# Kernel tuning notes

Hardware: AMD Instinct MI355X
Metric: run time of the kernel (lower is better)

The kernel has to match this reference:

```python
import jax, jax.numpy as jnp
import numpy as np

B, R, A, S, F, N = 2, 1, 16, 14, 1024, 512  # batch, num_rx, num_rx_ant, ofdm_symbols, fft_size, num_effective_sc
D = S * N  # flattened time-frequency dim that C acts on


def setup_inputs() -> dict:
    key = jax.random.key(0)
    k0, k1, k2, k3 = jax.random.split(key, 4)
    scale = 1.0 / np.sqrt(D).astype(np.float32)
    x_re = jax.random.normal(k0, (B, R, A, S, F), jnp.float32)
    x_im = jax.random.normal(k1, (B, R, A, S, F), jnp.float32)
    C_re = jax.random.normal(k2, (D, D), jnp.float32) * scale
    C_im = jax.random.normal(k3, (D, D), jnp.float32) * scale
    # unique, sorted effective-subcarrier indices (as in an OFDM ResourceGrid)
    sc_ind = jnp.asarray(np.sort(np.random.default_rng(0).choice(F, N, replace=False)), jnp.int32)
    return {"x_re": x_re, "x_im": x_im, "C_re": C_re, "C_im": C_im, "sc_ind": sc_ind}


def reference(x_re, x_im, C_re, C_im, sc_ind):
    x = jax.lax.complex(x_re, x_im)            # [B,R,A,S,F] complex64
    C = jax.lax.complex(C_re, C_im)            # [D,D]
    y = jnp.take(x, sc_ind, axis=-1)           # gather effective subcarriers -> [B,R,A,S,N]
    b, r, a, s, n = y.shape
    yf = y.reshape(b, r, a, s * n)             # flatten_last_dims(y, 2)
    # multiply_from_right with adjoint: yf @ C^H
    yf = jnp.einsum('brad,ed->brae', yf, jnp.conj(C))
    y = yf.reshape(b, r, a, s, n)
    # scatter back into full fft_size grid (unique indices -> set == scatter_nd on zeros)
    out = jnp.zeros((b, r, a, s, F), y.dtype).at[..., sc_ind].set(y)
    return jnp.stack([out.real, out.imag])     # [2,B,R,A,S,F] (real, imag)
```

## Files before the change

kernel.cpp:

```cpp
#include <hip/hip_runtime.h>
#include <hip/hip_bf16.h>

#define B_ 2
#define R_ 1
#define A_ 16
#define S_ 14
#define F_ 1024
#define N_ 512
#define D_ (S_*N_)
#define M_ (B_*R_*A_)
#define KK_ (2*D_)
#define BE 64
#define ETILES (D_/BE)

typedef __attribute__((ext_vector_type(8))) short bf16x8;
typedef __attribute__((ext_vector_type(4))) float f32x4;

static __device__ inline short f2bf(float f) {
    __hip_bfloat16 h = __float2bfloat16(f);
    return *reinterpret_cast<short*>(&h);
}
static __device__ inline float bf2f(short s) {
    unsigned int u = ((unsigned int)(unsigned short)s) << 16;
    return __uint_as_float(u);
}

#define LDSP(p) ((__attribute__((address_space(3))) void*)(p))
#define GLBP(p) ((const __attribute__((address_space(1))) void*)(p))

__global__ void prep_kernel(const float* __restrict__ xr, const float* __restrict__ xi,
                            const int* __restrict__ sc, short* __restrict__ Ap) {
    int idx = blockIdx.x * blockDim.x + threadIdx.x;
    if (idx >= 64 * KK_) return;
    int k = idx % KK_;
    int r = idx / KK_;
    int m = r & 31;
    int half = (k >= D_) ? 1 : 0;
    int d = half ? (k - D_) : k;
    int s = d >> 9;
    int n = d & 511;
    int f = sc[n];
    const float* base = (r < 32) ? (half ? xi : xr) : (half ? xr : xi);
    float v = base[(m * S_ + s) * F_ + f];
    if (r >= 32 && half) v = -v;
    Ap[((size_t)(k >> 3) * 64 + r) * 8 + (k & 7)] = f2bf(v);
}

__global__ void zero_kernel(float4* __restrict__ out, int n4) {
    int i = blockIdx.x * blockDim.x + threadIdx.x;
    if (i < n4) out[i] = make_float4(0.f, 0.f, 0.f, 0.f);
}

__global__ __launch_bounds__(256) void gemm_wasync(
    const short* __restrict__ Ap,
    const float* __restrict__ Cre, const float* __restrict__ Cim,
    short* __restrict__ part_all)
{
    constexpr int KSPLIT = 28;
    constexpr int KBLK = KK_ / KSPLIT;
    constexpr int NCH  = KBLK / 32;
    __shared__ float Bl[4][3][16 * 32];
    __shared__ short Al[4][3][64 * 32];

    const int etile = blockIdx.x;
    const int ks    = blockIdx.y;
    const int tid   = threadIdx.x;
    const int wave  = tid >> 6;
    const int lane  = tid & 63;
    const int l16   = lane & 15;
    const int kg    = lane >> 4;

    const float* Cp = (ks < 14) ? Cre : Cim;
    const int kc = (ks % 14) * KBLK;
    const int ka = ks * KBLK;

    const int U0 = lane, U1 = 64 + lane;
    const float* bsrc0 = Cp + (size_t)(etile * 64 + wave * 16 + (U0 >> 3)) * D_
                            + kc + ((U0 & 7) ^ ((U0 >> 3) & 7)) * 4;
    const float* bsrc1 = Cp + (size_t)(etile * 64 + wave * 16 + (U1 >> 3)) * D_
                            + kc + ((U1 & 7) ^ ((U1 >> 3) & 7)) * 4;
    const short* asrc = Ap + (size_t)(ka >> 3) * 512 + lane * 8;

#define WAITV(n) asm volatile("s_waitcnt vmcnt(" #n ")" ::: "memory")
#define STAGE(cc) do { \
        int bb = (cc) % 3; \
        __builtin_amdgcn_global_load_lds(GLBP(bsrc0 + (size_t)(cc) * 32), \
                                         LDSP(&Bl[wave][bb][lane * 4]), 16, 0, 0); \
        __builtin_amdgcn_global_load_lds(GLBP(bsrc1 + (size_t)(cc) * 32), \
                                         LDSP(&Bl[wave][bb][(64 + lane) * 4]), 16, 0, 0); \
        __builtin_amdgcn_global_load_lds(GLBP(asrc + (size_t)(cc) * 2048 + 0 * 512), \
                                         LDSP(&Al[wave][bb][lane * 8]), 16, 0, 0); \
        __builtin_amdgcn_global_load_lds(GLBP(asrc + (size_t)(cc) * 2048 + 1 * 512), \
                                         LDSP(&Al[wave][bb][(64 + lane) * 8]), 16, 0, 0); \
        __builtin_amdgcn_global_load_lds(GLBP(asrc + (size_t)(cc) * 2048 + 2 * 512), \
                                         LDSP(&Al[wave][bb][(128 + lane) * 8]), 16, 0, 0); \
        __builtin_amdgcn_global_load_lds(GLBP(asrc + (size_t)(cc) * 2048 + 3 * 512), \
                                         LDSP(&Al[wave][bb][(192 + lane) * 8]), 16, 0, 0); \
    } while (0)

    STAGE(0);
    STAGE(1);
    STAGE(2);

    f32x4 acc0 = {0.f,0.f,0.f,0.f}, acc1 = {0.f,0.f,0.f,0.f};
    f32x4 acc2 = {0.f,0.f,0.f,0.f}, acc3 = {0.f,0.f,0.f,0.f};

    const int swz  = l16 & 7;
    const int boff = l16 * 32;
    const int u0x = ((kg * 2 + 0) ^ swz) * 4;
    const int u1x = ((kg * 2 + 1) ^ swz) * 4;

    for (int c = 0; c < NCH; ++c) {
        if (c <= NCH - 3)      { WAITV(12); }
        else if (c == NCH - 2) { WAITV(6); }
        else                   { WAITV(0); }
        __builtin_amdgcn_sched_barrier(0);

        const int buf = c % 3;
        f32x4 b0 = *reinterpret_cast<const f32x4*>(&Bl[wave][buf][boff + u0x]);
        f32x4 b1 = *reinterpret_cast<const f32x4*>(&Bl[wave][buf][boff + u1x]);
        bf16x8 a0 = *reinterpret_cast<const bf16x8*>(&Al[wave][buf][(kg * 64 + 0 * 16 + l16) * 8]);
        bf16x8 a1 = *reinterpret_cast<const bf16x8*>(&Al[wave][buf][(kg * 64 + 1 * 16 + l16) * 8]);
        bf16x8 a2 = *reinterpret_cast<const bf16x8*>(&Al[wave][buf][(kg * 64 + 2 * 16 + l16) * 8]);
        bf16x8 a3 = *reinterpret_cast<const bf16x8*>(&Al[wave][buf][(kg * 64 + 3 * 16 + l16) * 8]);
        asm volatile("s_waitcnt lgkmcnt(0)" ::: "memory");
        __builtin_amdgcn_sched_barrier(0);

        if (c + 3 < NCH) STAGE(c + 3);
        __builtin_amdgcn_sched_barrier(0);

        bf16x8 bfv;
        bfv[0] = f2bf(b0.x); bfv[1] = f2bf(b0.y); bfv[2] = f2bf(b0.z); bfv[3] = f2bf(b0.w);
        bfv[4] = f2bf(b1.x); bfv[5] = f2bf(b1.y); bfv[6] = f2bf(b1.z); bfv[7] = f2bf(b1.w);
        acc0 = __builtin_amdgcn_mfma_f32_16x16x32_bf16(a0, bfv, acc0, 0, 0, 0);
        acc1 = __builtin_amdgcn_mfma_f32_16x16x32_bf16(a1, bfv, acc1, 0, 0, 0);
        acc2 = __builtin_amdgcn_mfma_f32_16x16x32_bf16(a2, bfv, acc2, 0, 0, 0);
        acc3 = __builtin_amdgcn_mfma_f32_16x16x32_bf16(a3, bfv, acc3, 0, 0, 0);
    }
#undef STAGE
#undef WAITV

    const int e_lane = etile * 64 + wave * 16 + l16;
    short* part = part_all + (size_t)ks * (64 * D_);
    #pragma unroll
    for (int mt = 0; mt < 4; ++mt) {
        f32x4 a = (mt == 0) ? acc0 : (mt == 1) ? acc1 : (mt == 2) ? acc2 : acc3;
        int rbase = mt * 16 + kg * 4;
        #pragma unroll
        for (int r = 0; r < 4; ++r)
            part[(size_t)(rbase + r) * D_ + e_lane] = f2bf(a[r]);
    }
}

template<int KSPLIT, int PARTIALS>
__global__ __launch_bounds__(256) void gemm_sync(
    const short* __restrict__ Ap,
    const float* __restrict__ Cre, const float* __restrict__ Cim,
    const int* __restrict__ sc,
    void* __restrict__ outp)
{
    constexpr int KBLK = KK_ / KSPLIT;
    constexpr int NCH  = KBLK / 32;
    __shared__ float Bls[3][64 * 32];
    __shared__ short Als[3][64 * 32];

    const int etile = blockIdx.x;
    const int ks    = blockIdx.y;
    const int tid   = threadIdx.x;
    const int wave  = tid >> 6;
    const int lane  = tid & 63;
    const int l16   = lane & 15;
    const int kg    = lane >> 4;

    const float* Cp = (ks < KSPLIT / 2) ? Cre : Cim;
    const int kc = (ks % (KSPLIT / 2)) * KBLK;
    const int ka = ks * KBLK;

    const float* bsrc[2];
    #pragma unroll
    for (int q = 0; q < 2; ++q) {
        int U = q * 256 + tid;
        int row = U >> 3;
        int u = (U & 7) ^ (row & 7);
        bsrc[q] = Cp + (size_t)(etile * BE + row) * D_ + kc + u * 4;
    }
    const short* asrc = Ap + ((size_t)(ka >> 3) * 64) * 8 + tid * 8;

#define STG(c) do { \
        int bf_ = (c) % 3; \
        __builtin_amdgcn_global_load_lds(GLBP(bsrc[0] + (size_t)(c) * 32), \
                                         LDSP(&Bls[bf_][(0 * 256 + tid) * 4]), 16, 0, 0); \
        __builtin_amdgcn_global_load_lds(GLBP(bsrc[1] + (size_t)(c) * 32), \
                                         LDSP(&Bls[bf_][(1 * 256 + tid) * 4]), 16, 0, 0); \
        __builtin_amdgcn_global_load_lds(GLBP(asrc + (size_t)(c) * 2048), \
                                         LDSP(&Als[bf_][tid * 8]), 16, 0, 0); \
    } while (0)

    STG(0);
    STG(1);

    f32x4 acc0 = {0.f,0.f,0.f,0.f}, acc1 = {0.f,0.f,0.f,0.f};
    f32x4 acc2 = {0.f,0.f,0.f,0.f}, acc3 = {0.f,0.f,0.f,0.f};

    const int row  = wave * 16 + l16;
    const int swz  = row & 7;
    const int boff = row * 32;
    const int u0 = ((kg * 2 + 0) ^ swz) * 4;
    const int u1 = ((kg * 2 + 1) ^ swz) * 4;

    for (int c = 0; c < NCH; ++c) {
        if (c < NCH - 1) asm volatile("s_waitcnt vmcnt(3)" ::: "memory");
        else             asm volatile("s_waitcnt vmcnt(0)" ::: "memory");
        __builtin_amdgcn_sched_barrier(0);
        __builtin_amdgcn_s_barrier();

        const int buf = c % 3;
        f32x4 b0 = *reinterpret_cast<const f32x4*>(&Bls[buf][boff + u0]);
        f32x4 b1 = *reinterpret_cast<const f32x4*>(&Bls[buf][boff + u1]);
        bf16x8 a0 = *reinterpret_cast<const bf16x8*>(&Als[buf][(kg * 64 + 0 * 16 + l16) * 8]);
        bf16x8 a1 = *reinterpret_cast<const bf16x8*>(&Als[buf][(kg * 64 + 1 * 16 + l16) * 8]);
        bf16x8 a2 = *reinterpret_cast<const bf16x8*>(&Als[buf][(kg * 64 + 2 * 16 + l16) * 8]);
        bf16x8 a3 = *reinterpret_cast<const bf16x8*>(&Als[buf][(kg * 64 + 3 * 16 + l16) * 8]);
        asm volatile("s_waitcnt lgkmcnt(0)" ::: "memory");
        __builtin_amdgcn_sched_barrier(0);
        __builtin_amdgcn_s_barrier();

        if (c + 2 < NCH) STG(c + 2);

        bf16x8 bfv;
        bfv[0] = f2bf(b0.x); bfv[1] = f2bf(b0.y); bfv[2] = f2bf(b0.z); bfv[3] = f2bf(b0.w);
        bfv[4] = f2bf(b1.x); bfv[5] = f2bf(b1.y); bfv[6] = f2bf(b1.z); bfv[7] = f2bf(b1.w);
        acc0 = __builtin_amdgcn_mfma_f32_16x16x32_bf16(a0, bfv, acc0, 0, 0, 0);
        acc1 = __builtin_amdgcn_mfma_f32_16x16x32_bf16(a1, bfv, acc1, 0, 0, 0);
        acc2 = __builtin_amdgcn_mfma_f32_16x16x32_bf16(a2, bfv, acc2, 0, 0, 0);
        acc3 = __builtin_amdgcn_mfma_f32_16x16x32_bf16(a3, bfv, acc3, 0, 0, 0);
    }
#undef STG

    const int e_lane = etile * BE + row;
    if (PARTIALS) {
        short* part = (short*)outp + (size_t)ks * (64 * D_);
        #pragma unroll
        for (int mt = 0; mt < 4; ++mt) {
            f32x4 a = (mt == 0) ? acc0 : (mt == 1) ? acc1 : (mt == 2) ? acc2 : acc3;
            int rbase = mt * 16 + kg * 4;
            #pragma unroll
            for (int r = 0; r < 4; ++r)
                part[(size_t)(rbase + r) * D_ + e_lane] = f2bf(a[r]);
        }
    } else {
        float* out = (float*)outp;
        int s = e_lane >> 9, n = e_lane & 511;
        int f = sc[n];
        #pragma unroll
        for (int mt = 0; mt < 4; ++mt) {
            f32x4 a = (mt == 0) ? acc0 : (mt == 1) ? acc1 : (mt == 2) ? acc2 : acc3;
            int rbase = mt * 16 + kg * 4;
            #pragma unroll
            for (int r = 0; r < 4; ++r) {
                int rr = rbase + r;
                int pp = rr >> 5, m = rr & 31;
                atomicAdd(&out[((pp * M_ + m) * S_ + s) * F_ + f], a[r]);
            }
        }
    }
}

template<int KSPLIT>
__global__ void reduce_kernel(const short* __restrict__ part, const int* __restrict__ sc,
                              float* __restrict__ out) {
    int t = blockIdx.x * blockDim.x + threadIdx.x;
    if (t >= 64 * D_ / 8) return;
    int base = t * 8;
    int e0 = base % D_;
    int r  = base / D_;
    float v[8] = {0.f,0.f,0.f,0.f,0.f,0.f,0.f,0.f};
    #pragma unroll
    for (int ksp = 0; ksp < KSPLIT; ++ksp) {
        bf16x8 x = *reinterpret_cast<const bf16x8*>(&part[(size_t)ksp * (64 * D_) + base]);
        #pragma unroll
        for (int j = 0; j < 8; ++j) v[j] += bf2f(x[j]);
    }
    int pp = r >> 5, m = r & 31, s = e0 >> 9, n0 = e0 & 511;
    float* ob = &out[((pp * M_ + m) * S_ + s) * F_];
    #pragma unroll
    for (int j = 0; j < 8; ++j) ob[sc[n0 + j]] = v[j];
}

extern "C" void kernel_launch(void* const* d_in, const int* in_sizes, int n_in,
                              void* d_out, int out_size, void* d_ws, size_t ws_size,
                              hipStream_t stream) {
    const float* xr  = (const float*)d_in[0];
    const float* xi  = (const float*)d_in[1];
    const float* Cre = (const float*)d_in[2];
    const float* Cim = (const float*)d_in[3];
    const int*   sc  = (const int*)d_in[4];
    float* out = (float*)d_out;

    short* Ap = (short*)d_ws;
    const size_t partOff = 2u * 1024u * 1024u;
    const size_t need28  = partOff + 28ull * 64 * D_ * 2;
    const size_t need16  = partOff + 16ull * 64 * D_ * 2;

    prep_kernel<<<dim3((64 * KK_ + 255) / 256), 256, 0, stream>>>(xr, xi, sc, Ap);
    zero_kernel<<<dim3((917504 / 4 + 255) / 256), 256, 0, stream>>>((float4*)out, 917504 / 4);

    const int rthreads = 64 * D_ / 8;
    if (ws_size >= need28) {
        short* part = (short*)((char*)d_ws + partOff);
        gemm_wasync<<<dim3(ETILES, 28), 256, 0, stream>>>(Ap, Cre, Cim, part);
        reduce_kernel<28><<<dim3((rthreads + 255) / 256), 256, 0, stream>>>(part, sc, out);
    } else if (ws_size >= need16) {
        short* part = (short*)((char*)d_ws + partOff);
        gemm_sync<16, 1><<<dim3(ETILES, 16), 256, 0, stream>>>(Ap, Cre, Cim, sc, part);
        reduce_kernel<16><<<dim3((rthreads + 255) / 256), 256, 0, stream>>>(part, sc, out);
    } else {
        gemm_sync<16, 0><<<dim3(ETILES, 16), 256, 0, stream>>>(Ap, Cre, Cim, sc, out);
    }
}
```

Baseline: 123.8 us.

## Replace LDS-staged split-K GEMM with register-prefetched GEMM and gather-based reduce

The main GEMM drops the global_load_lds staging through shared memory and instead prefetches C and A fragments straight into registers, several chunks deep. The K split goes from 28 to 14, halving the partial buffer traffic, and launch bounds ask for 2 blocks per CU. The reduce now writes the full output grid by looking up an inverse subcarrier map built by a new kernel, which removes the separate zero pass and the scattered writes. prep_kernel now reads each x element once and writes all four bf16 entries. Trade-offs: much higher register pressure from the prefetch arrays, fewer blocks in the GEMM grid, and gathered (non-vector) reads of the partials in the reduce.

```diff
diff --git a/kernel.cpp b/kernel.cpp
--- a/kernel.cpp
+++ b/kernel.cpp
@@ -31,19 +31,27 @@
 __global__ void prep_kernel(const float* __restrict__ xr, const float* __restrict__ xi,
                             const int* __restrict__ sc, short* __restrict__ Ap) {
     int idx = blockIdx.x * blockDim.x + threadIdx.x;
-    if (idx >= 64 * KK_) return;
-    int k = idx % KK_;
-    int r = idx / KK_;
-    int m = r & 31;
-    int half = (k >= D_) ? 1 : 0;
-    int d = half ? (k - D_) : k;
+    if (idx >= 32 * D_) return;
+    int d = idx % D_;
+    int m = idx / D_;
     int s = d >> 9;
     int n = d & 511;
     int f = sc[n];
-    const float* base = (r < 32) ? (half ? xi : xr) : (half ? xr : xi);
-    float v = base[(m * S_ + s) * F_ + f];
-    if (r >= 32 && half) v = -v;
-    Ap[((size_t)(k >> 3) * 64 + r) * 8 + (k & 7)] = f2bf(v);
+    float vr = xr[(m * S_ + s) * F_ + f];
+    float vi = xi[(m * S_ + s) * F_ + f];
+    int g1 = d >> 3, j = d & 7;
+    int g2 = (D_ + d) >> 3;
+    Ap[((size_t)g1 * 64 + m) * 8 + j]      = f2bf(vr);
+    Ap[((size_t)g1 * 64 + 32 + m) * 8 + j] = f2bf(vi);
+    Ap[((size_t)g2 * 64 + m) * 8 + j]      = f2bf(vi);
+    Ap[((size_t)g2 * 64 + 32 + m) * 8 + j] = f2bf(-vr);
+}
+
+__global__ void inv_kernel(const int* __restrict__ sc, int* __restrict__ inv) {
+    int t = threadIdx.x;
+    inv[t] = -1;
+    __syncthreads();
+    if (t < N_) inv[sc[t]] = t;
 }
 
 __global__ void zero_kernel(float4* __restrict__ out, int n4) {
@@ -51,16 +59,16 @@
     if (i < n4) out[i] = make_float4(0.f, 0.f, 0.f, 0.f);
 }
 
-__global__ __launch_bounds__(256) void gemm_wasync(
+__global__ __launch_bounds__(256, 2) void gemm_reg(
     const short* __restrict__ Ap,
     const float* __restrict__ Cre, const float* __restrict__ Cim,
     short* __restrict__ part_all)
 {
-    constexpr int KSPLIT = 28;
+    constexpr int KSPLIT = 14;
     constexpr int KBLK = KK_ / KSPLIT;
     constexpr int NCH  = KBLK / 32;
-    __shared__ float Bl[4][3][16 * 32];
-    __shared__ short Al[4][3][64 * 32];
+    constexpr int BD   = 5;
+    constexpr int AD   = 8;
 
     const int etile = blockIdx.x;
     const int ks    = blockIdx.y;
@@ -70,65 +78,51 @@
     const int l16   = lane & 15;
     const int kg    = lane >> 4;
 
-    const float* Cp = (ks < 14) ? Cre : Cim;
-    const int kc = (ks % 14) * KBLK;
+    const float* Cp = (ks < 7) ? Cre : Cim;
+    const int kc = (ks % 7) * KBLK;
     const int ka = ks * KBLK;
 
-    const int U0 = lane, U1 = 64 + lane;
-    const float* bsrc0 = Cp + (size_t)(etile * 64 + wave * 16 + (U0 >> 3)) * D_
-                            + kc + ((U0 & 7) ^ ((U0 >> 3) & 7)) * 4;
-    const float* bsrc1 = Cp + (size_t)(etile * 64 + wave * 16 + (U1 >> 3)) * D_
-                            + kc + ((U1 & 7) ^ ((U1 >> 3) & 7)) * 4;
-    const short* asrc = Ap + (size_t)(ka >> 3) * 512 + lane * 8;
-
-#define WAITV(n) asm volatile("s_waitcnt vmcnt(" #n ")" ::: "memory")
-#define STAGE(cc) do { \
-        int bb = (cc) % 3; \
-        __builtin_amdgcn_global_load_lds(GLBP(bsrc0 + (size_t)(cc) * 32), \
-                                         LDSP(&Bl[wave][bb][lane * 4]), 16, 0, 0); \
-        __builtin_amdgcn_global_load_lds(GLBP(bsrc1 + (size_t)(cc) * 32), \
-                                         LDSP(&Bl[wave][bb][(64 + lane) * 4]), 16, 0, 0); \
-        __builtin_amdgcn_global_load_lds(GLBP(asrc + (size_t)(cc) * 2048 + 0 * 512), \
-                                         LDSP(&Al[wave][bb][lane * 8]), 16, 0, 0); \
-        __builtin_amdgcn_global_load_lds(GLBP(asrc + (size_t)(cc) * 2048 + 1 * 512), \
-                                         LDSP(&Al[wave][bb][(64 + lane) * 8]), 16, 0, 0); \
-        __builtin_amdgcn_global_load_lds(GLBP(asrc + (size_t)(cc) * 2048 + 2 * 512), \
-                                         LDSP(&Al[wave][bb][(128 + lane) * 8]), 16, 0, 0); \
-        __builtin_amdgcn_global_load_lds(GLBP(asrc + (size_t)(cc) * 2048 + 3 * 512), \
-                                         LDSP(&Al[wave][bb][(192 + lane) * 8]), 16, 0, 0); \
-    } while (0)
-
-    STAGE(0);
-    STAGE(1);
-    STAGE(2);
+    const int e_lane = etile * BE + wave * 16 + l16;
+    const float* crow = Cp + (size_t)e_lane * D_ + kc + kg * 8;
+    const short* abase = Ap + (((size_t)(ka >> 3) + kg) * 64 + l16) * 8;
+
+    f32x4  breg[BD][2];
+    bf16x8 areg[AD][4];
+
+    #pragma unroll
+    for (int j = 0; j < AD; ++j)
+        #pragma unroll
+        for (int mt = 0; mt < 4; ++mt)
+            areg[j][mt] = *reinterpret_cast<const bf16x8*>(abase + (size_t)j * 2048 + mt * 128);
+    #pragma unroll
+    for (int j = 0; j < BD; ++j) {
+        breg[j][0] = *reinterpret_cast<const f32x4*>(crow + j * 32);
+        breg[j][1] = *reinterpret_cast<const f32x4*>(crow + j * 32 + 4);
+    }
+    __builtin_amdgcn_sched_barrier(0);
 
     f32x4 acc0 = {0.f,0.f,0.f,0.f}, acc1 = {0.f,0.f,0.f,0.f};
     f32x4 acc2 = {0.f,0.f,0.f,0.f}, acc3 = {0.f,0.f,0.f,0.f};
 
-    const int swz  = l16 & 7;
-    const int boff = l16 * 32;
-    const int u0x = ((kg * 2 + 0) ^ swz) * 4;
-    const int u1x = ((kg * 2 + 1) ^ swz) * 4;
-
+    #pragma unroll
     for (int c = 0; c < NCH; ++c) {
-        if (c <= NCH - 3)      { WAITV(12); }
-        else if (c == NCH - 2) { WAITV(6); }
-        else                   { WAITV(0); }
+        f32x4 b0 = breg[c % BD][0];
+        f32x4 b1 = breg[c % BD][1];
+        bf16x8 a0 = areg[c % AD][0];
+        bf16x8 a1 = areg[c % AD][1];
+        bf16x8 a2 = areg[c % AD][2];
+        bf16x8 a3 = areg[c % AD][3];
+        if (c + BD < NCH) {
+            breg[c % BD][0] = *reinterpret_cast<const f32x4*>(crow + (c + BD) * 32);
+            breg[c % BD][1] = *reinterpret_cast<const f32x4*>(crow + (c + BD) * 32 + 4);
+        }
+        if (c + AD < NCH) {
+            #pragma unroll
+            for (int mt = 0; mt < 4; ++mt)
+                areg[c % AD][mt] = *reinterpret_cast<const bf16x8*>(
+                    abase + (size_t)(c + AD) * 2048 + mt * 128);
+        }
         __builtin_amdgcn_sched_barrier(0);
-
-        const int buf = c % 3;
-        f32x4 b0 = *reinterpret_cast<const f32x4*>(&Bl[wave][buf][boff + u0x]);
-        f32x4 b1 = *reinterpret_cast<const f32x4*>(&Bl[wave][buf][boff + u1x]);
-        bf16x8 a0 = *reinterpret_cast<const bf16x8*>(&Al[wave][buf][(kg * 64 + 0 * 16 + l16) * 8]);
-        bf16x8 a1 = *reinterpret_cast<const bf16x8*>(&Al[wave][buf][(kg * 64 + 1 * 16 + l16) * 8]);
-        bf16x8 a2 = *reinterpret_cast<const bf16x8*>(&Al[wave][buf][(kg * 64 + 2 * 16 + l16) * 8]);
-        bf16x8 a3 = *reinterpret_cast<const bf16x8*>(&Al[wave][buf][(kg * 64 + 3 * 16 + l16) * 8]);
-        asm volatile("s_waitcnt lgkmcnt(0)" ::: "memory");
-        __builtin_amdgcn_sched_barrier(0);
-
-        if (c + 3 < NCH) STAGE(c + 3);
-        __builtin_amdgcn_sched_barrier(0);
-
         bf16x8 bfv;
         bfv[0] = f2bf(b0.x); bfv[1] = f2bf(b0.y); bfv[2] = f2bf(b0.z); bfv[3] = f2bf(b0.w);
         bfv[4] = f2bf(b1.x); bfv[5] = f2bf(b1.y); bfv[6] = f2bf(b1.z); bfv[7] = f2bf(b1.w);
@@ -137,10 +131,7 @@
         acc2 = __builtin_amdgcn_mfma_f32_16x16x32_bf16(a2, bfv, acc2, 0, 0, 0);
         acc3 = __builtin_amdgcn_mfma_f32_16x16x32_bf16(a3, bfv, acc3, 0, 0, 0);
     }
-#undef STAGE
-#undef WAITV
-
-    const int e_lane = etile * 64 + wave * 16 + l16;
+
     short* part = part_all + (size_t)ks * (64 * D_);
     #pragma unroll
     for (int mt = 0; mt < 4; ++mt) {
@@ -152,12 +143,37 @@
     }
 }
 
-template<int KSPLIT, int PARTIALS>
+__global__ void reduce_full(const short* __restrict__ part, const int* __restrict__ inv,
+                            float* __restrict__ out) {
+    int t = blockIdx.x * blockDim.x + threadIdx.x;
+    if (t >= 896 * 128) return;
+    int fg  = t % 128;
+    int row = t / 128;
+    int s   = row % S_;
+    int rm  = row / S_;
+    int f0  = fg * 8;
+    int nn[8];
+    #pragma unroll
+    for (int j = 0; j < 8; ++j) nn[j] = inv[f0 + j];
+    float v[8] = {0.f,0.f,0.f,0.f,0.f,0.f,0.f,0.f};
+    #pragma unroll
+    for (int ksp = 0; ksp < 14; ++ksp) {
+        const short* p = part + ((size_t)ksp * 64 + rm) * D_ + s * 512;
+        #pragma unroll
+        for (int j = 0; j < 8; ++j)
+            if (nn[j] >= 0) v[j] += bf2f(p[nn[j]]);
+    }
+    float* ob = &out[(size_t)row * F_ + f0];
+    #pragma unroll
+    for (int j = 0; j < 8; ++j) ob[j] = v[j];
+}
+
+template<int KSPLIT>
 __global__ __launch_bounds__(256) void gemm_sync(
     const short* __restrict__ Ap,
     const float* __restrict__ Cre, const float* __restrict__ Cim,
     const int* __restrict__ sc,
-    void* __restrict__ outp)
+    float* __restrict__ out)
 {
     constexpr int KBLK = KK_ / KSPLIT;
     constexpr int NCH  = KBLK / 32;
@@ -238,53 +254,19 @@
 #undef STG
 
     const int e_lane = etile * BE + row;
-    if (PARTIALS) {
-        short* part = (short*)outp + (size_t)ks * (64 * D_);
+    int s = e_lane >> 9, n = e_lane & 511;
+    int f = sc[n];
+    #pragma unroll
+    for (int mt = 0; mt < 4; ++mt) {
+        f32x4 a = (mt == 0) ? acc0 : (mt == 1) ? acc1 : (mt == 2) ? acc2 : acc3;
+        int rbase = mt * 16 + kg * 4;
         #pragma unroll
-        for (int mt = 0; mt < 4; ++mt) {
-            f32x4 a = (mt == 0) ? acc0 : (mt == 1) ? acc1 : (mt == 2) ? acc2 : acc3;
-            int rbase = mt * 16 + kg * 4;
-            #pragma unroll
-            for (int r = 0; r < 4; ++r)
-                part[(size_t)(rbase + r) * D_ + e_lane] = f2bf(a[r]);
+        for (int r = 0; r < 4; ++r) {
+            int rr = rbase + r;
+            int pp = rr >> 5, m = rr & 31;
+            atomicAdd(&out[((pp * M_ + m) * S_ + s) * F_ + f], a[r]);
         }
-    } else {
-        float* out = (float*)outp;
-        int s = e_lane >> 9, n = e_lane & 511;
-        int f = sc[n];
-        #pragma unroll
-        for (int mt = 0; mt < 4; ++mt) {
-            f32x4 a = (mt == 0) ? acc0 : (mt == 1) ? acc1 : (mt == 2) ? acc2 : acc3;
-            int rbase = mt * 16 + kg * 4;
-            #pragma unroll
-            for (int r = 0; r < 4; ++r) {
-                int rr = rbase + r;
-                int pp = rr >> 5, m = rr & 31;
-                atomicAdd(&out[((pp * M_ + m) * S_ + s) * F_ + f], a[r]);
-            }
-        }
-    }
-}
-
-template<int KSPLIT>
-__global__ void reduce_kernel(const short* __restrict__ part, const int* __restrict__ sc,
-                              float* __restrict__ out) {
-    int t = blockIdx.x * blockDim.x + threadIdx.x;
-    if (t >= 64 * D_ / 8) return;
-    int base = t * 8;
-    int e0 = base % D_;
-    int r  = base / D_;
-    float v[8] = {0.f,0.f,0.f,0.f,0.f,0.f,0.f,0.f};
-    #pragma unroll
-    for (int ksp = 0; ksp < KSPLIT; ++ksp) {
-        bf16x8 x = *reinterpret_cast<const bf16x8*>(&part[(size_t)ksp * (64 * D_) + base]);
-        #pragma unroll
-        for (int j = 0; j < 8; ++j) v[j] += bf2f(x[j]);
-    }
-    int pp = r >> 5, m = r & 31, s = e0 >> 9, n0 = e0 & 511;
-    float* ob = &out[((pp * M_ + m) * S_ + s) * F_];
-    #pragma unroll
-    for (int j = 0; j < 8; ++j) ob[sc[n0 + j]] = v[j];
+    }
 }
 
 extern "C" void kernel_launch(void* const* d_in, const int* in_sizes, int n_in,
@@ -298,23 +280,21 @@
     float* out = (float*)d_out;
 
     short* Ap = (short*)d_ws;
-    const size_t partOff = 2u * 1024u * 1024u;
-    const size_t need28  = partOff + 28ull * 64 * D_ * 2;
-    const size_t need16  = partOff + 16ull * 64 * D_ * 2;
-
-    prep_kernel<<<dim3((64 * KK_ + 255) / 256), 256, 0, stream>>>(xr, xi, sc, Ap);
-    zero_kernel<<<dim3((917504 / 4 + 255) / 256), 256, 0, stream>>>((float4*)out, 917504 / 4);
-
-    const int rthreads = 64 * D_ / 8;
-    if (ws_size >= need28) {
+    const size_t invOff  = 2u * 1024u * 1024u;
+    const size_t partOff = invOff + 4096;
+    const size_t partBytes = 14ull * 64 * D_ * 2;
+    const bool ok = ws_size >= partOff + partBytes;
+
+    prep_kernel<<<dim3((32 * D_ + 255) / 256), 256, 0, stream>>>(xr, xi, sc, Ap);
+
+    if (ok) {
+        int* inv = (int*)((char*)d_ws + invOff);
         short* part = (short*)((char*)d_ws + partOff);
-        gemm_wasync<<<dim3(ETILES, 28), 256, 0, stream>>>(Ap, Cre, Cim, part);
-        reduce_kernel<28><<<dim3((rthreads + 255) / 256), 256, 0, stream>>>(part, sc, out);
-    } else if (ws_size >= need16) {
-        short* part = (short*)((char*)d_ws + partOff);
-        gemm_sync<16, 1><<<dim3(ETILES, 16), 256, 0, stream>>>(Ap, Cre, Cim, sc, part);
-        reduce_kernel<16><<<dim3((rthreads + 255) / 256), 256, 0, stream>>>(part, sc, out);
+        inv_kernel<<<1, 1024, 0, stream>>>(sc, inv);
+        gemm_reg<<<dim3(ETILES, 14), 256, 0, stream>>>(Ap, Cre, Cim, part);
+        reduce_full<<<dim3((896 * 128 + 255) / 256), 256, 0, stream>>>(part, inv, out);
     } else {
-        gemm_sync<16, 0><<<dim3(ETILES, 16), 256, 0, stream>>>(Ap, Cre, Cim, sc, out);
-    }
-}
+        zero_kernel<<<dim3((917504 / 4 + 255) / 256), 256, 0, stream>>>((float4*)out, 917504 / 4);
+        gemm_sync<16><<<dim3(ETILES, 16), 256, 0, stream>>>(Ap, Cre, Cim, sc, out);
+    }
+}
```

Result: slower. 150.1 us (+21.2%).
